# Kernel optimization log

Measured on AMD Instinct MI355X. Metric: run time of the kernel, lower is better.

Reference implementation:

```python
import jax, jax.numpy as jnp
import numpy as np

HEADS = 16
HEAD_DIM = 128
LAMBDA_INIT = 0.8
RMS_EPS = 1.1920928955078125e-07  # torch.finfo(float32).eps (RMSNorm eps=None default)


def setup_inputs() -> dict:
    key = jax.random.key(0)
    ks = jax.random.split(key, 9)
    b, s, d = 2, 2048, 2048
    x = jax.random.normal(ks[0], (b, s, d), dtype=jnp.float32)
    # torch Linear weights are (out_features, in_features); apply as x @ W.T
    wq = jax.random.normal(ks[1], (d, d), dtype=jnp.float32) * 0.02
    wk = jax.random.normal(ks[2], (d, d), dtype=jnp.float32) * 0.02
    wv = jax.random.normal(ks[3], (d, d), dtype=jnp.float32) * 0.02
    wo = jax.random.normal(ks[4], (d, d), dtype=jnp.float32) * 0.02
    # lambda vectors scaled small so exp(dot) stays finite
    lambda_q1 = jax.random.normal(ks[5], (HEAD_DIM,), dtype=jnp.float32) * 0.1
    lambda_q2 = jax.random.normal(ks[6], (HEAD_DIM,), dtype=jnp.float32) * 0.1
    lambda_k1 = jax.random.normal(ks[7], (HEAD_DIM,), dtype=jnp.float32) * 0.1
    lambda_k2 = jax.random.normal(ks[8], (HEAD_DIM,), dtype=jnp.float32) * 0.1
    return {"x": x, "wq": wq, "wk": wk, "wv": wv, "wo": wo,
            "lambda_q1": lambda_q1, "lambda_q2": lambda_q2,
            "lambda_k1": lambda_k1, "lambda_k2": lambda_k2}


def reference(x, wq, wk, wv, wo, lambda_q1, lambda_q2, lambda_k1, lambda_k2):
    b, s, d = x.shape
    h, hd = HEADS, HEAD_DIM
    # projections -> (b, h, s, hd)
    q = (x @ wq.T).reshape(b, s, h, hd).transpose(0, 2, 1, 3)
    k = (x @ wk.T).reshape(b, s, h, hd).transpose(0, 2, 1, 3)
    v = (x @ wv.T).reshape(b, s, h, hd).transpose(0, 2, 1, 3)
    q1, q2 = jnp.split(q, 2, axis=-1)
    k1, k2 = jnp.split(k, 2, axis=-1)
    # NOTE: source scales by sqrt(full head_dim), not the chunked dim
    scale = 1.0 / jnp.sqrt(jnp.float32(hd))
    a1 = jax.nn.softmax(jnp.einsum('bhqd,bhkd->bhqk', q1, k1) * scale, axis=-1)
    a2 = jax.nn.softmax(jnp.einsum('bhqd,bhkd->bhqk', q2, k2) * scale, axis=-1)
    lam = jnp.exp(jnp.dot(lambda_q1, lambda_k1)) - jnp.exp(jnp.dot(lambda_q2, lambda_k2)) + LAMBDA_INIT
    out = jnp.einsum('bhqk,bhkd->bhqd', a1 - lam * a2, v)  # (b,h,s,hd)
    # per-head RMSNorm (no affine) scaled by (1 - lambda_init)
    rms = jnp.sqrt(jnp.mean(out * out, axis=-1, keepdims=True) + RMS_EPS)
    normed = out / rms * (1.0 - LAMBDA_INIT)
    # faithful to torch: cat over heads on dim 1 -> (b, h*s, hd),
    # transpose(1,2) -> (b, hd, h*s), contiguous view -> (b, s, d)
    t = normed.reshape(b, h * s, hd).transpose(0, 2, 1).reshape(b, s, d)
    return t @ wo.T
```

## Files before the change

kernel.cpp:

```cpp
#include <hip/hip_runtime.h>
#include <hip/hip_bf16.h>
#include <cstdint>
#include <cstddef>

typedef __attribute__((ext_vector_type(8))) short short8;
typedef __attribute__((ext_vector_type(4))) short short4v;
typedef __attribute__((ext_vector_type(4))) float f4;
typedef __attribute__((ext_vector_type(4))) int i4;

typedef union { unsigned int w[4]; short8 s; } pk8_t;

#define MFMA16(a, b, c) __builtin_amdgcn_mfma_f32_16x16x32_bf16((a), (b), (c), 0, 0, 0)

__device__ __forceinline__ float bf2f(unsigned short u) {
    union { unsigned int i; float f; } v; v.i = ((unsigned int)u) << 16; return v.f;
}
__device__ __forceinline__ unsigned short f2bf(float f) {
    union { float f; unsigned int i; } v; v.f = f;
    unsigned int x = v.i;
    x += 0x7fffu + ((x >> 16) & 1u);
    return (unsigned short)(x >> 16);
}
__device__ __forceinline__ i4 pack8(const float* p) {
    f4 v0 = *(const f4*)p;
    f4 v1 = *(const f4*)(p + 4);
    unsigned int w0 = (unsigned int)f2bf(v0[0]) | ((unsigned int)f2bf(v0[1]) << 16);
    unsigned int w1 = (unsigned int)f2bf(v0[2]) | ((unsigned int)f2bf(v0[3]) << 16);
    unsigned int w2 = (unsigned int)f2bf(v1[0]) | ((unsigned int)f2bf(v1[1]) << 16);
    unsigned int w3 = (unsigned int)f2bf(v1[2]) | ((unsigned int)f2bf(v1[3]) << 16);
    i4 r; r[0] = (int)w0; r[1] = (int)w1; r[2] = (int)w2; r[3] = (int)w3; return r;
}
__device__ __forceinline__ void g2l16(const unsigned short* g, unsigned short* l) {
    __builtin_amdgcn_global_load_lds(
        (const __attribute__((address_space(1))) unsigned int*)g,
        (__attribute__((address_space(3))) unsigned int*)l,
        16, 0, 0);
}

static constexpr int S = 2048;
static constexpr int D = 2048;
static constexpr int H = 16;
static constexpr int HD = 128;
static constexpr int B = 2;

__global__ void detect_kernel(const unsigned short* __restrict__ w,
                              const void* __restrict__ lq1, const void* __restrict__ lq2,
                              const void* __restrict__ lk1, const void* __restrict__ lk2,
                              int* __restrict__ ctrl) {
    const int lane = threadIdx.x;
    int hits = 0;
    for (int j = 0; j < 4; j++) {
        unsigned short u = w[lane * 4 + j];
        hits += (((u >> 7) & 0xFF) >= 134) ? 1 : 0;
    }
    for (int m = 1; m <= 32; m <<= 1) hits += __shfl_xor(hits, m, 64);
    const int flag = (hits >= 16) ? 1 : 0;

    float d1 = 0.f, d2 = 0.f;
    for (int t = 0; t < 2; t++) {
        int e = lane + t * 64;
        float q1v, k1v, q2v, k2v;
        if (flag) {
            q1v = ((const float*)lq1)[e]; k1v = ((const float*)lk1)[e];
            q2v = ((const float*)lq2)[e]; k2v = ((const float*)lk2)[e];
        } else {
            q1v = bf2f(((const unsigned short*)lq1)[e]); k1v = bf2f(((const unsigned short*)lk1)[e]);
            q2v = bf2f(((const unsigned short*)lq2)[e]); k2v = bf2f(((const unsigned short*)lk2)[e]);
        }
        d1 += q1v * k1v; d2 += q2v * k2v;
    }
    for (int m = 1; m <= 32; m <<= 1) { d1 += __shfl_xor(d1, m, 64); d2 += __shfl_xor(d2, m, 64); }
    if (lane == 0) {
        ctrl[0] = flag;
        ctrl[1] = __float_as_int(__expf(d1) - __expf(d2) + 0.8f);
    }
}

__global__ __launch_bounds__(256) void conv_kernel(const void* __restrict__ src,
                                                   unsigned short* __restrict__ dst,
                                                   int n, const int* __restrict__ ctrl) {
    int i = (blockIdx.x * 256 + threadIdx.x) * 8;
    if (i >= n) return;
    if (ctrl[0]) *(i4*)&dst[i] = pack8(&((const float*)src)[i]);
    else         *(i4*)&dst[i] = *(const i4*)&((const unsigned short*)src)[i];
}

__global__ __launch_bounds__(256) void proj_kernel(
    const unsigned short* __restrict__ X,
    const unsigned short* __restrict__ Wq, const unsigned short* __restrict__ Wk,
    const unsigned short* __restrict__ Wv,
    unsigned short* __restrict__ Qb,
    unsigned short* __restrict__ Kb,
    unsigned short* __restrict__ Vt)
{
    const int zm = blockIdx.z;
    const unsigned short* __restrict__ W = (zm == 0) ? Wq : ((zm == 1) ? Wk : Wv);
    const int bm = blockIdx.x, bn = blockIdx.y;
    const int K = D;

    __shared__ __align__(16) unsigned short As[128 * 32];
    __shared__ __align__(16) unsigned short Bs[128 * 32];

    const int tid  = threadIdx.x;
    const int lane = tid & 63;
    const int wave = tid >> 6;
    const int quad = lane >> 4;
    const int l16  = lane & 15;
    const int wm   = (wave >> 1) * 64;
    const int wn   = (wave & 1) * 64;
    const int r0   = tid >> 2;
    const int koff = (tid & 3) * 8;

    f4 acc[4][4] = {};

    for (int k0 = 0; k0 < K; k0 += 32) {
        __syncthreads();
        g2l16(&X[(size_t)(bm * 128 + r0) * K + k0 + koff],
              (unsigned short*)((char*)As + wave * 1024));
        g2l16(&X[(size_t)(bm * 128 + r0 + 64) * K + k0 + koff],
              (unsigned short*)((char*)As + wave * 1024 + 4096));
        g2l16(&W[(size_t)(bn * 128 + r0) * K + k0 + koff],
              (unsigned short*)((char*)Bs + wave * 1024));
        g2l16(&W[(size_t)(bn * 128 + r0 + 64) * K + k0 + koff],
              (unsigned short*)((char*)Bs + wave * 1024 + 4096));
        __syncthreads();

        short8 a[4], b[4];
        #pragma unroll
        for (int i = 0; i < 4; i++) {
            a[i] = *(const short8*)&As[(wm + i * 16 + l16) * 32 + quad * 8];
            b[i] = *(const short8*)&Bs[(wn + i * 16 + l16) * 32 + quad * 8];
        }
        #pragma unroll
        for (int i = 0; i < 4; i++)
            #pragma unroll
            for (int j = 0; j < 4; j++)
                acc[i][j] = MFMA16(a[i], b[j], acc[i][j]);
    }

    for (int i = 0; i < 4; i++)
        for (int j = 0; j < 4; j++)
            for (int reg = 0; reg < 4; reg++) {
                int row = bm * 128 + wm + i * 16 + quad * 4 + reg;
                int col = bn * 128 + wn + j * 16 + l16;
                int b_idx = row >> 11, s0 = row & (S - 1);
                int h0 = col >> 7, e = col & (HD - 1);
                unsigned short val = f2bf(acc[i][j][reg]);
                if (zm == 2) {
                    Vt[(((size_t)(b_idx * H + h0)) * HD + e) * S + s0] = val;
                } else {
                    unsigned short* O = (zm == 0) ? Qb : Kb;
                    O[(((size_t)(b_idx * H + h0)) * S + s0) * HD + e] = val;
                }
            }
}

__global__ __launch_bounds__(256, 2) void attn_kernel(
    const unsigned short* __restrict__ Qb,
    const unsigned short* __restrict__ Kb,
    const unsigned short* __restrict__ Vt,
    const int* __restrict__ ctrl,
    unsigned short* __restrict__ Nm)
{
    const int idx = blockIdx.x + (blockIdx.y << 5) + (blockIdx.z << 9);
    const int swz = ((idx & 7) << 7) + (idx >> 3);
    const int qb = swz & 31;
    const int h  = (swz >> 5) & 15;
    const int b  = swz >> 9;

    const unsigned short* __restrict__ q  = Qb + ((size_t)(b * H + h)) * S * HD;
    const unsigned short* __restrict__ k  = Kb + ((size_t)(b * H + h)) * S * HD;
    const unsigned short* __restrict__ vt = Vt + ((size_t)(b * H + h)) * HD * S;
    const float lam = __int_as_float(ctrl[1]);

    const int tid  = threadIdx.x;
    const int lane = tid & 63;
    const int wave = tid >> 6;
    const int quad = lane >> 4;
    const int l16  = lane & 15;
    const int row0 = qb * 64 + wave * 16;

    short8 aq1[2], aq2[2];
    #pragma unroll
    for (int t = 0; t < 2; t++) {
        aq1[t] = *(const short8*)&q[((size_t)(row0 + l16)) * HD + t * 32 + quad * 8];
        aq2[t] = *(const short8*)&q[((size_t)(row0 + l16)) * HD + 64 + t * 32 + quad * 8];
    }

    float l1 = 0.f, l2 = 0.f;
    f4 o1[8] = {}, o2[8] = {};
    const float scale2 = 0.08838834764831845f * 1.4426950408889634f;

    #define LOADK(key0, kf)                                                              \
        {                                                                                \
            _Pragma("unroll") for (int tile = 0; tile < 2; tile++)                       \
            _Pragma("unroll") for (int v = 0; v < 2; v++)                                \
            _Pragma("unroll") for (int t = 0; t < 2; t++)                                \
                kf[tile][v][t] = *(const short8*)&k[(size_t)((key0) + 2 * l16 + tile) * HD \
                                                    + v * 64 + t * 32 + quad * 8];       \
        }
    #define LOADV(key0, vf)                                                              \
        {                                                                                \
            _Pragma("unroll") for (int f = 0; f < 8; f++)                                \
                vf[f] = *(const short8*)&vt[(size_t)(f * 16 + l16) * S + (key0) + quad * 8]; \
        }
    #define BODY(kf, vf)                                                                 \
        {                                                                                \
            f4 s1[2], s2[2];                                                             \
            _Pragma("unroll") for (int tile = 0; tile < 2; tile++) {                     \
                s1[tile] = (f4){};  s2[tile] = (f4){};                                   \
                _Pragma("unroll") for (int t = 0; t < 2; t++) {                          \
                    s1[tile] = MFMA16(kf[tile][0][t], aq1[t], s1[tile]);                 \
                    s2[tile] = MFMA16(kf[tile][1][t], aq2[t], s2[tile]);                 \
                }                                                                        \
            }                                                                            \
            float p1[2][4], p2[2][4];                                                    \
            _Pragma("unroll") for (int tile = 0; tile < 2; tile++)                       \
            _Pragma("unroll") for (int r = 0; r < 4; r++) {                              \
                p1[tile][r] = __builtin_amdgcn_exp2f(s1[tile][r] * scale2);              \
                p2[tile][r] = __builtin_amdgcn_exp2f(s2[tile][r] * scale2);              \
            }                                                                            \
            l1 += ((p1[0][0] + p1[0][1]) + (p1[0][2] + p1[0][3]))                        \
                + ((p1[1][0] + p1[1][1]) + (p1[1][2] + p1[1][3]));                       \
            l2 += ((p2[0][0] + p2[0][1]) + (p2[0][2] + p2[0][3]))                        \
                + ((p2[1][0] + p2[1][1]) + (p2[1][2] + p2[1][3]));                       \
            pk8_t pa1, pa2;                                                              \
            _Pragma("unroll") for (int m = 0; m < 4; m++) {                              \
                asm("v_cvt_pk_bf16_f32 %0, %1, %2"                                       \
                    : "=v"(pa1.w[m]) : "v"(p1[0][m]), "v"(p1[1][m]));                    \
                asm("v_cvt_pk_bf16_f32 %0, %1, %2"                                       \
                    : "=v"(pa2.w[m]) : "v"(p2[0][m]), "v"(p2[1][m]));                    \
            }                                                                            \
            _Pragma("unroll") for (int f = 0; f < 8; f++) {                              \
                o1[f] = MFMA16(pa1.s, vf[f], o1[f]);                                     \
                o2[f] = MFMA16(pa2.s, vf[f], o2[f]);                                     \
            }                                                                            \
        }

    short8 kA[2][2][2], kB[2][2][2];
    short8 vA[8], vB[8];
    LOADK(0, kA); LOADV(0, vA);

    for (int key0 = 0; key0 < S; key0 += 64) {
        LOADK(key0 + 32, kB); LOADV(key0 + 32, vB);
        BODY(kA, vA);
        int nx = (key0 + 64 < S) ? key0 + 64 : 0;
        LOADK(nx, kA); LOADV(nx, vA);
        BODY(kB, vB);
    }
    #undef LOADK
    #undef LOADV
    #undef BODY

    l1 += __shfl_xor(l1, 16, 64); l1 += __shfl_xor(l1, 32, 64);
    l2 += __shfl_xor(l2, 16, 64); l2 += __shfl_xor(l2, 32, 64);

    float il1[4], il2[4];
    #pragma unroll
    for (int r = 0; r < 4; r++) {
        il1[r] = 1.0f / __shfl(l1, quad * 4 + r, 64);
        il2[r] = lam  / __shfl(l2, quad * 4 + r, 64);
    }

    float ssq[4] = {};
    #pragma unroll
    for (int f = 0; f < 8; f++)
        #pragma unroll
        for (int r = 0; r < 4; r++) {
            float fin = o1[f][r] * il1[r] - o2[f][r] * il2[r];
            o1[f][r] = fin;
            ssq[r] += fin * fin;
        }
    #pragma unroll
    for (int r = 0; r < 4; r++)
        for (int mask = 1; mask <= 8; mask <<= 1)
            ssq[r] += __shfl_xor(ssq[r], mask, 64);

    for (int r = 0; r < 4; r++) {
        float rms = sqrtf(ssq[r] * (1.0f / 128.0f) + 1.1920928955078125e-07f);
        float sc = 0.2f / rms;
        int s0 = row0 + quad * 4 + r;
        for (int f = 0; f < 8; f++) {
            int e = f * 16 + l16;
            Nm[((size_t)b * D + (e * H + h)) * S + s0] = f2bf(o1[f][r] * sc);
        }
    }
}

__global__ __launch_bounds__(256) void out_kernel(
    const unsigned short* __restrict__ Nm,
    const unsigned short* __restrict__ Wo,
    const int* __restrict__ ctrl,
    void* __restrict__ Out)
{
    const int flag = ctrl[0];
    const int bz = blockIdx.z;
    const unsigned short* __restrict__ A = Nm + (size_t)bz * D * S;
    const int K = S;
    const int bm = blockIdx.x, bn = blockIdx.y;

    __shared__ __align__(16) unsigned short As[128 * 32];
    __shared__ __align__(16) unsigned short Bs[128 * 32];

    const int tid  = threadIdx.x;
    const int lane = tid & 63;
    const int wave = tid >> 6;
    const int quad = lane >> 4;
    const int l16  = lane & 15;
    const int wm   = (wave >> 1) * 64;
    const int wn   = (wave & 1) * 64;
    const int r0   = tid >> 2;
    const int koff = (tid & 3) * 8;

    f4 acc[4][4] = {};

    for (int k0 = 0; k0 < K; k0 += 32) {
        __syncthreads();
        g2l16(&A[(size_t)(bm * 128 + r0) * K + k0 + koff],
              (unsigned short*)((char*)As + wave * 1024));
        g2l16(&A[(size_t)(bm * 128 + r0 + 64) * K + k0 + koff],
              (unsigned short*)((char*)As + wave * 1024 + 4096));
        g2l16(&Wo[(size_t)(bn * 128 + r0) * K + k0 + koff],
              (unsigned short*)((char*)Bs + wave * 1024));
        g2l16(&Wo[(size_t)(bn * 128 + r0 + 64) * K + k0 + koff],
              (unsigned short*)((char*)Bs + wave * 1024 + 4096));
        __syncthreads();

        short8 a[4], b[4];
        #pragma unroll
        for (int i = 0; i < 4; i++) {
            a[i] = *(const short8*)&As[(wm + i * 16 + l16) * 32 + quad * 8];
            b[i] = *(const short8*)&Bs[(wn + i * 16 + l16) * 32 + quad * 8];
        }
        #pragma unroll
        for (int i = 0; i < 4; i++)
            #pragma unroll
            for (int j = 0; j < 4; j++)
                acc[i][j] = MFMA16(a[i], b[j], acc[i][j]);
    }

    for (int i = 0; i < 4; i++)
        for (int j = 0; j < 4; j++)
            for (int reg = 0; reg < 4; reg++) {
                int row = bm * 128 + wm + i * 16 + quad * 4 + reg;
                int col = bn * 128 + wn + j * 16 + l16;
                size_t idx = (size_t)bz * S * D + (size_t)row * D + col;
                if (flag) ((float*)Out)[idx] = acc[i][j][reg];
                else      ((unsigned short*)Out)[idx] = f2bf(acc[i][j][reg]);
            }
}

static constexpr size_t NEED_BYTES = 256 + 56ull * 1024 * 1024 * 2;
static void* g_extra = nullptr;

extern "C" void kernel_launch(void* const* d_in, const int* in_sizes, int n_in,
                              void* d_out, int out_size, void* d_ws, size_t ws_size,
                              hipStream_t stream) {
    const void* x   = d_in[0];
    const void* wq  = d_in[1];
    const void* wk  = d_in[2];
    const void* wv  = d_in[3];
    const void* wo  = d_in[4];
    const void* lq1 = d_in[5];
    const void* lq2 = d_in[6];
    const void* lk1 = d_in[7];
    const void* lk2 = d_in[8];

    char* base;
    if (ws_size >= NEED_BYTES) {
        base = (char*)d_ws;
    } else {
        if (!g_extra) (void)hipMalloc(&g_extra, NEED_BYTES);
        base = g_extra ? (char*)g_extra : (char*)d_ws;
    }

    int* ctrl = (int*)base;
    unsigned short* pw = (unsigned short*)(base + 256);
    const size_t NX = (size_t)B * S * D;
    const size_t NW = (size_t)D * D;
    const size_t NH = (size_t)B * H * S * HD;
    unsigned short* Xc  = pw;  pw += NX;
    unsigned short* Wqc = pw;  pw += NW;
    unsigned short* Wkc = pw;  pw += NW;
    unsigned short* Wvc = pw;  pw += NW;
    unsigned short* Woc = pw;  pw += NW;
    unsigned short* Qb  = pw;  pw += NH;
    unsigned short* Kb  = pw;  pw += NH;
    unsigned short* Vt  = pw;  pw += NH;
    unsigned short* Nm  = pw;

    detect_kernel<<<1, 64, 0, stream>>>((const unsigned short*)wq, lq1, lq2, lk1, lk2, ctrl);

    conv_kernel<<<(int)(NX / 2048), 256, 0, stream>>>(x,  Xc,  (int)NX, ctrl);
    conv_kernel<<<(int)(NW / 2048), 256, 0, stream>>>(wq, Wqc, (int)NW, ctrl);
    conv_kernel<<<(int)(NW / 2048), 256, 0, stream>>>(wk, Wkc, (int)NW, ctrl);
    conv_kernel<<<(int)(NW / 2048), 256, 0, stream>>>(wv, Wvc, (int)NW, ctrl);
    conv_kernel<<<(int)(NW / 2048), 256, 0, stream>>>(wo, Woc, (int)NW, ctrl);

    dim3 g1(32, 16, 3);
    proj_kernel<<<g1, 256, 0, stream>>>(Xc, Wqc, Wkc, Wvc, Qb, Kb, Vt);

    dim3 g2(S / 64, H, B);
    attn_kernel<<<g2, 256, 0, stream>>>(Qb, Kb, Vt, ctrl, Nm);

    dim3 g3(16, 16, 2);
    out_kernel<<<g3, 256, 0, stream>>>(Nm, Woc, ctrl, d_out);
}
```

Before: 866.2 us.

## Split differential attention into two sequential passes to cut register pressure

The fused loop that computed both softmax branches (q1/k1 and q2/k2) together is replaced by two separate passes over all keys, each with its own accumulator and K half. This halves live accumulator and K-fragment registers per pass, which may raise occupancy or avoid spills. The cost is that the V tiles are streamed from memory twice and the key loop runs twice.

```diff
diff --git a/kernel.cpp b/kernel.cpp
--- a/kernel.cpp
+++ b/kernel.cpp
@@ -180,77 +180,74 @@
     const int l16  = lane & 15;
     const int row0 = qb * 64 + wave * 16;
 
-    short8 aq1[2], aq2[2];
-    #pragma unroll
-    for (int t = 0; t < 2; t++) {
-        aq1[t] = *(const short8*)&q[((size_t)(row0 + l16)) * HD + t * 32 + quad * 8];
-        aq2[t] = *(const short8*)&q[((size_t)(row0 + l16)) * HD + 64 + t * 32 + quad * 8];
-    }
-
-    float l1 = 0.f, l2 = 0.f;
-    f4 o1[8] = {}, o2[8] = {};
     const float scale2 = 0.08838834764831845f * 1.4426950408889634f;
 
-    #define LOADK(key0, kf)                                                              \
+    #define LOADKD(key0, kf, DOFF)                                                       \
         {                                                                                \
             _Pragma("unroll") for (int tile = 0; tile < 2; tile++)                       \
-            _Pragma("unroll") for (int v = 0; v < 2; v++)                                \
-            _Pragma("unroll") for (int t = 0; t < 2; t++)                                \
-                kf[tile][v][t] = *(const short8*)&k[(size_t)((key0) + 2 * l16 + tile) * HD \
-                                                    + v * 64 + t * 32 + quad * 8];       \
+            _Pragma("unroll") for (int t_ = 0; t_ < 2; t_++)                             \
+                kf[tile][t_] = *(const short8*)&k[(size_t)((key0) + 2 * l16 + tile) * HD \
+                                                  + (DOFF) + t_ * 32 + quad * 8];        \
         }
     #define LOADV(key0, vf)                                                              \
         {                                                                                \
             _Pragma("unroll") for (int f = 0; f < 8; f++)                                \
                 vf[f] = *(const short8*)&vt[(size_t)(f * 16 + l16) * S + (key0) + quad * 8]; \
         }
-    #define BODY(kf, vf)                                                                 \
+    #define BODYV(kf, vf, aqv, oacc, lsum)                                               \
         {                                                                                \
-            f4 s1[2], s2[2];                                                             \
+            f4 s[2];                                                                     \
             _Pragma("unroll") for (int tile = 0; tile < 2; tile++) {                     \
-                s1[tile] = (f4){};  s2[tile] = (f4){};                                   \
-                _Pragma("unroll") for (int t = 0; t < 2; t++) {                          \
-                    s1[tile] = MFMA16(kf[tile][0][t], aq1[t], s1[tile]);                 \
-                    s2[tile] = MFMA16(kf[tile][1][t], aq2[t], s2[tile]);                 \
-                }                                                                        \
+                s[tile] = (f4){};                                                        \
+                _Pragma("unroll") for (int t_ = 0; t_ < 2; t_++)                         \
+                    s[tile] = MFMA16(kf[tile][t_], aqv[t_], s[tile]);                    \
             }                                                                            \
-            float p1[2][4], p2[2][4];                                                    \
+            float p[2][4];                                                               \
             _Pragma("unroll") for (int tile = 0; tile < 2; tile++)                       \
-            _Pragma("unroll") for (int r = 0; r < 4; r++) {                              \
-                p1[tile][r] = __builtin_amdgcn_exp2f(s1[tile][r] * scale2);              \
-                p2[tile][r] = __builtin_amdgcn_exp2f(s2[tile][r] * scale2);              \
+            _Pragma("unroll") for (int r = 0; r < 4; r++)                                \
+                p[tile][r] = __builtin_amdgcn_exp2f(s[tile][r] * scale2);                \
+            lsum += ((p[0][0] + p[0][1]) + (p[0][2] + p[0][3]))                          \
+                  + ((p[1][0] + p[1][1]) + (p[1][2] + p[1][3]));                         \
+            pk8_t pa;                                                                    \
+            _Pragma("unroll") for (int m = 0; m < 4; m++)                                \
+                asm("v_cvt_pk_bf16_f32 %0, %1, %2"                                       \
+                    : "=v"(pa.w[m]) : "v"(p[0][m]), "v"(p[1][m]));                       \
+            _Pragma("unroll") for (int f = 0; f < 8; f++)                                \
+                oacc[f] = MFMA16(pa.s, vf[f], oacc[f]);                                  \
+        }
+    #define PASS(DOFF, aqv, oacc, lsum)                                                  \
+        {                                                                                \
+            short8 kA[2][2], kB[2][2], vA[8], vB[8];                                     \
+            LOADKD(0, kA, DOFF); LOADV(0, vA);                                           \
+            for (int key0 = 0; key0 < S; key0 += 64) {                                   \
+                LOADKD(key0 + 32, kB, DOFF); LOADV(key0 + 32, vB);                       \
+                BODYV(kA, vA, aqv, oacc, lsum);                                          \
+                int nx = (key0 + 64 < S) ? key0 + 64 : 0;                                \
+                LOADKD(nx, kA, DOFF); LOADV(nx, vA);                                     \
+                BODYV(kB, vB, aqv, oacc, lsum);                                          \
             }                                                                            \
-            l1 += ((p1[0][0] + p1[0][1]) + (p1[0][2] + p1[0][3]))                        \
-                + ((p1[1][0] + p1[1][1]) + (p1[1][2] + p1[1][3]));                       \
-            l2 += ((p2[0][0] + p2[0][1]) + (p2[0][2] + p2[0][3]))                        \
-                + ((p2[1][0] + p2[1][1]) + (p2[1][2] + p2[1][3]));                       \
-            pk8_t pa1, pa2;                                                              \
-            _Pragma("unroll") for (int m = 0; m < 4; m++) {                              \
-                asm("v_cvt_pk_bf16_f32 %0, %1, %2"                                       \
-                    : "=v"(pa1.w[m]) : "v"(p1[0][m]), "v"(p1[1][m]));                    \
-                asm("v_cvt_pk_bf16_f32 %0, %1, %2"                                       \
-                    : "=v"(pa2.w[m]) : "v"(p2[0][m]), "v"(p2[1][m]));                    \
-            }                                                                            \
-            _Pragma("unroll") for (int f = 0; f < 8; f++) {                              \
-                o1[f] = MFMA16(pa1.s, vf[f], o1[f]);                                     \
-                o2[f] = MFMA16(pa2.s, vf[f], o2[f]);                                     \
-            }                                                                            \
-        }
-
-    short8 kA[2][2][2], kB[2][2][2];
-    short8 vA[8], vB[8];
-    LOADK(0, kA); LOADV(0, vA);
-
-    for (int key0 = 0; key0 < S; key0 += 64) {
-        LOADK(key0 + 32, kB); LOADV(key0 + 32, vB);
-        BODY(kA, vA);
-        int nx = (key0 + 64 < S) ? key0 + 64 : 0;
-        LOADK(nx, kA); LOADV(nx, vA);
-        BODY(kB, vB);
-    }
-    #undef LOADK
+        }
+
+    short8 aq1[2];
+    #pragma unroll
+    for (int t = 0; t < 2; t++)
+        aq1[t] = *(const short8*)&q[((size_t)(row0 + l16)) * HD + t * 32 + quad * 8];
+    f4 o1[8] = {};
+    float l1 = 0.f;
+    PASS(0, aq1, o1, l1);
+
+    short8 aq2[2];
+    #pragma unroll
+    for (int t = 0; t < 2; t++)
+        aq2[t] = *(const short8*)&q[((size_t)(row0 + l16)) * HD + 64 + t * 32 + quad * 8];
+    f4 o2[8] = {};
+    float l2 = 0.f;
+    PASS(64, aq2, o2, l2);
+
+    #undef LOADKD
     #undef LOADV
-    #undef BODY
+    #undef BODYV
+    #undef PASS
 
     l1 += __shfl_xor(l1, 16, 64); l1 += __shfl_xor(l1, 32, 64);
     l2 += __shfl_xor(l2, 16, 64); l2 += __shfl_xor(l2, 32, 64);
```

Measured after the change: 1.025 ms. 1.18x slower.
